# Optimization experiments

Measured on AMD Instinct MI355X. Metric: run time of the kernel, lower is better.

## Reference

```python
import jax, jax.numpy as jnp
import numpy as np

NUM_EXPERTS = 8
EMBED_DIM = 1024
EXPERT_DIM = 2048
TOP_K = 2
B, T = 2, 1024


def setup_inputs() -> dict:
    key = jax.random.key(0)
    ks = jax.random.split(key, 7)
    std = 0.02
    return {
        "x": jax.random.normal(ks[0], (B, T, EMBED_DIM), dtype=jnp.float32),
        "gate_inputs": jax.random.normal(ks[1], (B, T, EMBED_DIM), dtype=jnp.float32),
        "gate_kernel": jax.random.normal(ks[2], (EMBED_DIM, NUM_EXPERTS), dtype=jnp.float32) * std,
        "per_expert_scale": jnp.ones((NUM_EXPERTS,), dtype=jnp.float32),
        "gate_proj_w": jax.random.normal(ks[3], (NUM_EXPERTS, EMBED_DIM, EXPERT_DIM), dtype=jnp.float32) * std,
        "up_proj_w": jax.random.normal(ks[4], (NUM_EXPERTS, EMBED_DIM, EXPERT_DIM), dtype=jnp.float32) * std,
        "down_proj_w": jax.random.normal(ks[5], (NUM_EXPERTS, EXPERT_DIM, EMBED_DIM), dtype=jnp.float32) * std,
    }


def reference(x, gate_inputs, gate_kernel, per_expert_scale,
              gate_proj_w, up_proj_w, down_proj_w):
    Bb, Tt, D = x.shape
    x_flat = x.reshape(Bb * Tt, D)          # [t, e]
    g_flat = gate_inputs.reshape(Bb * Tt, D)

    logits = jnp.dot(g_flat, gate_kernel)   # [t, n]
    topk_logits, topk_idx = jax.lax.top_k(logits, TOP_K)  # [t, k]
    weights = jax.nn.sigmoid(topk_logits)   # [t, k]

    # Dense all-expert projections (as in the original module)
    gate_out = jnp.einsum('te,ned->tnd', x_flat, gate_proj_w)  # [t, n, d]
    up_out = jnp.einsum('te,ned->tnd', x_flat, up_proj_w)
    act = jax.nn.gelu(gate_out) * up_out
    expert_out = jnp.einsum('tnd,nde->tne', act, down_proj_w)  # [t, n, e]
    expert_out = expert_out * per_expert_scale[None, :, None]

    mask = jax.nn.one_hot(topk_idx, NUM_EXPERTS, dtype=expert_out.dtype)  # [t, k, n]
    selected = jnp.einsum('tkn,tne->tke', mask, expert_out)               # [t, k, e]
    out = jnp.einsum('tk,tke->te', weights, selected)                     # [t, e]
    return out.reshape(Bb, Tt, D)
```

## Files before the change

### kernel.cpp

```cpp
#include <hip/hip_runtime.h>
#include <math.h>
#include <stdint.h>

#define NE 8
#define ED 1024
#define FD 2048
#define NTOK 2048
#define BM 128
#define BN 128
#define BK 64

typedef unsigned short u16;
typedef unsigned int u32;
typedef __attribute__((ext_vector_type(4))) float f32x4;
typedef __attribute__((ext_vector_type(8))) short s16x8;
typedef __attribute__((ext_vector_type(4))) unsigned int u32v4;


__device__ __forceinline__ u16 f2bf(float f) {
    u32 u = __builtin_bit_cast(u32, f);
    u32 r = u + 0x7fffu + ((u >> 16) & 1u);
    return (u16)(r >> 16);
}

typedef __attribute__((address_space(1))) const void gvoid_t;
typedef __attribute__((address_space(3))) void lvoid_t;

__device__ __forceinline__ void gload16(const void* g, void* l) {
    __builtin_amdgcn_global_load_lds((gvoid_t*)g, (lvoid_t*)l, 16, 0, 0);
}


#define WS_CNT 0u
#define WS_OFF 64u
#define WS_TOK 256u
#define WS_WT  65792u
#define WS_XB  131328u
#define WS_WG  (8u << 20)
#define WS_WU  41943040u
#define WS_WD  75497472u
#define WS_ACT 109051904u
#define WS_NEED 130023424u


__global__ __launch_bounds__(256) void k_router(
        const float* __restrict__ gin, const float* __restrict__ gk,
        int* __restrict__ cnt, int* __restrict__ tok, float* __restrict__ wl) {
    int lane = threadIdx.x & 63;
    int t = (blockIdx.x * 256 + threadIdx.x) >> 6;
    if (t >= NTOK) return;
    const float* row = gin + (size_t)t * ED;
    float acc[NE];
#pragma unroll
    for (int e = 0; e < NE; e++) acc[e] = 0.f;
    for (int i = lane; i < ED; i += 64) {
        float v = row[i];
        const float* g = gk + i * NE;
#pragma unroll
        for (int e = 0; e < NE; e++) acc[e] = fmaf(v, g[e], acc[e]);
    }
#pragma unroll
    for (int e = 0; e < NE; e++) {
#pragma unroll
        for (int off = 32; off > 0; off >>= 1)
            acc[e] += __shfl_down(acc[e], off, 64);
    }
    if (lane == 0) {
        int b0 = 0; float v0 = acc[0];
#pragma unroll
        for (int e = 1; e < NE; e++) if (acc[e] > v0) { v0 = acc[e]; b0 = e; }
        int b1 = -1; float v1 = -3.4e38f;
#pragma unroll
        for (int e = 0; e < NE; e++) if (e != b0 && acc[e] > v1) { v1 = acc[e]; b1 = e; }
        float w0 = 1.f / (1.f + __expf(-v0));
        float w1 = 1.f / (1.f + __expf(-v1));
        int p0 = atomicAdd(&cnt[b0], 1);
        tok[b0 * NTOK + p0] = t; wl[b0 * NTOK + p0] = w0;
        int p1 = atomicAdd(&cnt[b1], 1);
        tok[b1 * NTOK + p1] = t; wl[b1 * NTOK + p1] = w1;
    }
}

__global__ void k_scan(const int* __restrict__ cnt, int* __restrict__ off) {
    if (threadIdx.x == 0 && blockIdx.x == 0) {
        int a = 0;
#pragma unroll
        for (int e = 0; e < NE; e++) { off[e] = a; a += (cnt[e] + 127) & ~127; }
        off[NE] = a;
    }
}


__global__ __launch_bounds__(256) void k_cvtx(const float4* __restrict__ x, uint2* __restrict__ xb) {
    int i = blockIdx.x * 256 + threadIdx.x;
    float4 v = x[i];
    uint2 o;
    o.x = (u32)f2bf(v.x) | ((u32)f2bf(v.y) << 16);
    o.y = (u32)f2bf(v.z) | ((u32)f2bf(v.w) << 16);
    xb[i] = o;
}


__global__ __launch_bounds__(256, 4) void k_cvtw(
        const float* __restrict__ wgf, const float* __restrict__ wuf, const float* __restrict__ wdf,
        u16* __restrict__ og, u16* __restrict__ ou, u16* __restrict__ od) {
    int b = blockIdx.x;
    const float* src; u16* dst; int ROW; int e, s;
    if (b < 1024)      { src = wgf; dst = og; ROW = FD; e = b >> 7;  s = b & 127; }
    else if (b < 2048) { int b2 = b - 1024; src = wuf; dst = ou; ROW = FD; e = b2 >> 7; s = b2 & 127; }
    else               { int b2 = b - 2048; src = wdf; dst = od; ROW = ED; e = b2 >> 8; s = b2 & 255; }
    int kc = s >> 3, g = s & 7;
    int rpe = (ROW == FD) ? ED : FD;
    const float* base = src + (size_t)e * (size_t)rpe * ROW + (size_t)s * 8 * ROW;

    __shared__ u32 sl[4 * 2052];
    int tid = threadIdx.x;
    int chunks = ROW >> 10;

    for (int kp = 0; kp < 4; kp++) {
        const float* r0 = base + (size_t)(2 * kp) * ROW;
        for (int ch = 0; ch < chunks; ch++) {
            int n4 = ch * 256 + tid;
            float4 f0 = *((const float4*)r0 + n4);
            float4 f1 = *((const float4*)(r0 + ROW) + n4);
            u32v4 w;
            w.x = (u32)f2bf(f0.x) | ((u32)f2bf(f1.x) << 16);
            w.y = (u32)f2bf(f0.y) | ((u32)f2bf(f1.y) << 16);
            w.z = (u32)f2bf(f0.z) | ((u32)f2bf(f1.z) << 16);
            w.w = (u32)f2bf(f0.w) | ((u32)f2bf(f1.w) << 16);
            *(u32v4*)(sl + kp * 2052 + 4 * n4) = w;
        }
    }
    __syncthreads();

    int iters = ROW >> 8;
    for (int it = 0; it < iters; it++) {
        int n = it * 256 + tid;
        u32v4 w;
        w.x = sl[0 * 2052 + n];
        w.y = sl[1 * 2052 + n];
        w.z = sl[2 * 2052 + n];
        w.w = sl[3 * 2052 + n];
        int nt = n >> 7;
        int img = (ROW == FD) ? ((e * 16 + nt) * 16 + kc)
                              : ((e * 8 + nt) * 32 + kc);
        u16* ob = dst + (size_t)img * 8192 + (size_t)g * 1024 + (size_t)(n & 127) * 8;
        *(u32v4*)ob = w;
    }
}


__global__ __launch_bounds__(256, 2) void k_passA(
        const u16* __restrict__ xb, const u16* __restrict__ wg, const u16* __restrict__ wu,
        const int* __restrict__ cnt, const int* __restrict__ off,
        const int* __restrict__ tok, u16* __restrict__ act) {
    int e = blockIdx.z, mt = blockIdx.y, nt = blockIdx.x;
    int c = cnt[e];
    if (mt * BM >= c) return;
    int rmax = c - mt * BM; if (rmax > BM) rmax = BM;

    __shared__ u16 sA[BM * BK];
    __shared__ u16 sBg[BN * BK];
    __shared__ u16 sBu[BN * BK];

    int tid = threadIdx.x;
    int lane = tid & 63, wv = tid >> 6;
    int wm = wv >> 1, wn = wv & 1;
    int col = lane & 15, quad = lane >> 4;
    int swz = col & 7;

    f32x4 zero = {0.f, 0.f, 0.f, 0.f};
    f32x4 ag[4][4], au[4][4];
#pragma unroll
    for (int i = 0; i < 4; i++)
#pragma unroll
        for (int j = 0; j < 4; j++) { ag[i][j] = zero; au[i][j] = zero; }

    int am = tid >> 1, ah = tid & 1;
    int ridx = mt * BM + am; if (ridx > c - 1) ridx = c - 1;
    int trow = tok[e * NTOK + ridx];
    const u16* asrc = xb + (size_t)trow * ED + ah * 32;
    u16* adst = sA + am * BK;

    const u16* gg = wg + ((size_t)(e * 16 + nt) * 16) * 8192;
    const u16* gu = wu + ((size_t)(e * 16 + nt) * 16) * 8192;
    const u16* bsrc0 = (wv < 2 ? gg : gu);
    int bhalf = (wv & 1) * 4096;
    u16* bdst = (wv < 2 ? sBg : sBu) + bhalf;

    for (int kc = 0; kc < 16; kc++) {
        __syncthreads();
        const u16* bs = bsrc0 + (size_t)kc * 8192 + bhalf + lane * 8;
#pragma unroll
        for (int i = 0; i < 8; i++)
            gload16(bs + i * 512, bdst + i * 512);
        const u16* as = asrc + kc * 64;
#pragma unroll
        for (int j = 0; j < 4; j++) {
            int pg = (ah * 4 + j) ^ (am & 7);
            *(u32v4*)(adst + pg * 8) = *(const u32v4*)(as + j * 8);
        }
        __syncthreads();
#pragma unroll
        for (int st = 0; st < 2; st++) {
            int g4 = st * 4 + quad;
            int aoff = (g4 ^ swz) * 8;
            s16x8 af[4];
#pragma unroll
            for (int mf = 0; mf < 4; mf++)
                af[mf] = *(const s16x8*)(sA + (wm * 64 + mf * 16 + col) * BK + aoff);
#pragma unroll
            for (int nf = 0; nf < 4; nf++) {
                int boff = g4 * 1024 + (wn * 64 + nf * 16 + col) * 8;
                s16x8 bg = *(const s16x8*)(sBg + boff);
                s16x8 bu = *(const s16x8*)(sBu + boff);
#pragma unroll
                for (int mf = 0; mf < 4; mf++) {
                    ag[mf][nf] = __builtin_amdgcn_mfma_f32_16x16x32_bf16(af[mf], bg, ag[mf][nf], 0, 0, 0);
                    au[mf][nf] = __builtin_amdgcn_mfma_f32_16x16x32_bf16(af[mf], bu, au[mf][nf], 0, 0, 0);
                }
            }
        }
    }

    int tile = (off[e] >> 7) + mt;
    u16* ab = act + (size_t)tile * (32 * 8192);
#pragma unroll
    for (int mf = 0; mf < 4; mf++) {
#pragma unroll
        for (int reg = 0; reg < 4; reg++) {
            int m = wm * 64 + mf * 16 + quad * 4 + reg;
            if (m < rmax) {
#pragma unroll
                for (int nf = 0; nf < 4; nf++) {
                    float gv = ag[mf][nf][reg];
                    float uv = au[mf][nf][reg];
                    float z = 0.7978845608028654f * (gv + 0.044715f * gv * gv * gv);
                    float ez = __expf(-2.f * fabsf(z));
                    float th = (1.f - ez) / (1.f + ez);
                    th = (z < 0.f) ? -th : th;
                    float a = 0.5f * gv * (1.f + th) * uv;
                    int ng = nt * 128 + wn * 64 + nf * 16 + col;
                    ab[(size_t)(ng >> 6) * 8192 + (size_t)((ng >> 3) & 7) * 1024
                       + (size_t)m * 8 + (ng & 7)] = f2bf(a);
                }
            }
        }
    }
}


__global__ __launch_bounds__(256, 3) void k_passB(
        const u16* __restrict__ act, const u16* __restrict__ wd,
        const int* __restrict__ cnt, const int* __restrict__ off,
        const int* __restrict__ tok, const float* __restrict__ wl,
        const float* __restrict__ scale, float* __restrict__ out) {
    int e = blockIdx.z, mt = blockIdx.y, nt = blockIdx.x;
    int c = cnt[e];
    if (mt * BM >= c) return;
    int rmax = c - mt * BM; if (rmax > BM) rmax = BM;

    __shared__ u16 sA[BM * BK];
    __shared__ u16 sB[BN * BK];

    int tid = threadIdx.x;
    int lane = tid & 63, wv = tid >> 6;
    int wm = wv >> 1, wn = wv & 1;
    int col = lane & 15, quad = lane >> 4;

    f32x4 zero = {0.f, 0.f, 0.f, 0.f};
    f32x4 acc[4][4];
#pragma unroll
    for (int i = 0; i < 4; i++)
#pragma unroll
        for (int j = 0; j < 4; j++) acc[i][j] = zero;

    int tile = (off[e] >> 7) + mt;
    const u16* ga = act + (size_t)tile * (32 * 8192);
    const u16* gb = wd + ((size_t)(e * 8 + nt) * 32) * 8192;
    const u16* src0 = (wv < 2 ? ga : gb);
    int shalf = (wv & 1) * 4096;
    u16* dst0 = (wv < 2 ? sA : sB) + shalf;

    for (int kc = 0; kc < 32; kc++) {
        __syncthreads();
        const u16* s = src0 + (size_t)kc * 8192 + shalf + lane * 8;
#pragma unroll
        for (int i = 0; i < 8; i++)
            gload16(s + i * 512, dst0 + i * 512);
        __syncthreads();
#pragma unroll
        for (int st = 0; st < 2; st++) {
            int g4 = st * 4 + quad;
            int abase = g4 * 1024;
            s16x8 af[4];
#pragma unroll
            for (int mf = 0; mf < 4; mf++)
                af[mf] = *(const s16x8*)(sA + abase + (wm * 64 + mf * 16 + col) * 8);
#pragma unroll
            for (int nf = 0; nf < 4; nf++) {
                s16x8 bf = *(const s16x8*)(sB + abase + (wn * 64 + nf * 16 + col) * 8);
#pragma unroll
                for (int mf = 0; mf < 4; mf++)
                    acc[mf][nf] = __builtin_amdgcn_mfma_f32_16x16x32_bf16(af[mf], bf, acc[mf][nf], 0, 0, 0);
            }
        }
    }

    float sc = scale[e];
    int lbase = e * NTOK + mt * BM;
#pragma unroll
    for (int mf = 0; mf < 4; mf++) {
#pragma unroll
        for (int reg = 0; reg < 4; reg++) {
            int m = wm * 64 + mf * 16 + quad * 4 + reg;
            if (m < rmax) {
                int t = tok[lbase + m];
                float w = wl[lbase + m] * sc;
                float* orow = out + (size_t)t * ED + nt * 128 + wn * 64 + col;
#pragma unroll
                for (int nf = 0; nf < 4; nf++)
                    atomicAdd(orow + nf * 16, acc[mf][nf][reg] * w);
            }
        }
    }
}


extern "C" void kernel_launch(void* const* d_in, const int* in_sizes, int n_in,
                              void* d_out, int out_size, void* d_ws, size_t ws_size,
                              hipStream_t stream) {
    const float* x   = (const float*)d_in[0];
    const float* gin = (const float*)d_in[1];
    const float* gk  = (const float*)d_in[2];
    const float* sc  = (const float*)d_in[3];
    const float* wgf = (const float*)d_in[4];
    const float* wuf = (const float*)d_in[5];
    const float* wdf = (const float*)d_in[6];
    float* out = (float*)d_out;

    if (ws_size < (size_t)WS_NEED) {
        hipMemsetAsync(d_out, 0, (size_t)out_size * sizeof(float), stream);
        return;
    }

    char* ws = (char*)d_ws;
    int*   cnt = (int*)(ws + WS_CNT);
    int*   off = (int*)(ws + WS_OFF);
    int*   tok = (int*)(ws + WS_TOK);
    float* wl  = (float*)(ws + WS_WT);
    u16*   xb  = (u16*)(ws + WS_XB);
    u16*   og  = (u16*)(ws + WS_WG);
    u16*   ou  = (u16*)(ws + WS_WU);
    u16*   od  = (u16*)(ws + WS_WD);
    u16*   act = (u16*)(ws + WS_ACT);

    hipMemsetAsync(cnt, 0, 64, stream);
    hipMemsetAsync(d_out, 0, (size_t)out_size * sizeof(float), stream);

    k_router<<<dim3(512), dim3(256), 0, stream>>>(gin, gk, cnt, tok, wl);
    k_scan<<<dim3(1), dim3(64), 0, stream>>>(cnt, off);
    k_cvtx<<<dim3(2048), dim3(256), 0, stream>>>((const float4*)x, (uint2*)xb);
    k_cvtw<<<dim3(4096), dim3(256), 0, stream>>>(wgf, wuf, wdf, og, ou, od);
    k_passA<<<dim3(16, 16, NE), dim3(256), 0, stream>>>(xb, og, ou, cnt, off, tok, act);
    k_passB<<<dim3(8, 16, NE), dim3(256), 0, stream>>>(act, od, cnt, off, tok, wl, sc, out);
}
```

Before: 429.2 us.

## Fuse router and conversions into one prep kernel, overlap down-weight conversion with passA

Merges the router, x conversion and gate/up weight conversion kernels into a single k_prep launch, which cuts launch count and tail gaps between them. The down-projection weight conversion moves into extra blocks of k_passA (grid z doubled), so it runs alongside the gate/up GEMM instead of before it. The cost is shared LDS sizing and branch divergence across block roles, and conversion blocks may compete with GEMM blocks for occupancy and bandwidth.

```diff
diff --git a/kernel.cpp b/kernel.cpp
--- a/kernel.cpp
+++ b/kernel.cpp
@@ -42,45 +42,6 @@
 #define WS_ACT 109051904u
 #define WS_NEED 130023424u
 
-
-__global__ __launch_bounds__(256) void k_router(
-        const float* __restrict__ gin, const float* __restrict__ gk,
-        int* __restrict__ cnt, int* __restrict__ tok, float* __restrict__ wl) {
-    int lane = threadIdx.x & 63;
-    int t = (blockIdx.x * 256 + threadIdx.x) >> 6;
-    if (t >= NTOK) return;
-    const float* row = gin + (size_t)t * ED;
-    float acc[NE];
-#pragma unroll
-    for (int e = 0; e < NE; e++) acc[e] = 0.f;
-    for (int i = lane; i < ED; i += 64) {
-        float v = row[i];
-        const float* g = gk + i * NE;
-#pragma unroll
-        for (int e = 0; e < NE; e++) acc[e] = fmaf(v, g[e], acc[e]);
-    }
-#pragma unroll
-    for (int e = 0; e < NE; e++) {
-#pragma unroll
-        for (int off = 32; off > 0; off >>= 1)
-            acc[e] += __shfl_down(acc[e], off, 64);
-    }
-    if (lane == 0) {
-        int b0 = 0; float v0 = acc[0];
-#pragma unroll
-        for (int e = 1; e < NE; e++) if (acc[e] > v0) { v0 = acc[e]; b0 = e; }
-        int b1 = -1; float v1 = -3.4e38f;
-#pragma unroll
-        for (int e = 0; e < NE; e++) if (e != b0 && acc[e] > v1) { v1 = acc[e]; b1 = e; }
-        float w0 = 1.f / (1.f + __expf(-v0));
-        float w1 = 1.f / (1.f + __expf(-v1));
-        int p0 = atomicAdd(&cnt[b0], 1);
-        tok[b0 * NTOK + p0] = t; wl[b0 * NTOK + p0] = w0;
-        int p1 = atomicAdd(&cnt[b1], 1);
-        tok[b1 * NTOK + p1] = t; wl[b1 * NTOK + p1] = w1;
-    }
-}
-
 __global__ void k_scan(const int* __restrict__ cnt, int* __restrict__ off) {
     if (threadIdx.x == 0 && blockIdx.x == 0) {
         int a = 0;
@@ -91,79 +52,156 @@
 }
 
 
-__global__ __launch_bounds__(256) void k_cvtx(const float4* __restrict__ x, uint2* __restrict__ xb) {
-    int i = blockIdx.x * 256 + threadIdx.x;
-    float4 v = x[i];
-    uint2 o;
-    o.x = (u32)f2bf(v.x) | ((u32)f2bf(v.y) << 16);
-    o.y = (u32)f2bf(v.z) | ((u32)f2bf(v.w) << 16);
-    xb[i] = o;
-}
-
-
-__global__ __launch_bounds__(256, 4) void k_cvtw(
-        const float* __restrict__ wgf, const float* __restrict__ wuf, const float* __restrict__ wdf,
-        u16* __restrict__ og, u16* __restrict__ ou, u16* __restrict__ od) {
-    int b = blockIdx.x;
-    const float* src; u16* dst; int ROW; int e, s;
-    if (b < 1024)      { src = wgf; dst = og; ROW = FD; e = b >> 7;  s = b & 127; }
-    else if (b < 2048) { int b2 = b - 1024; src = wuf; dst = ou; ROW = FD; e = b2 >> 7; s = b2 & 127; }
-    else               { int b2 = b - 2048; src = wdf; dst = od; ROW = ED; e = b2 >> 8; s = b2 & 255; }
-    int kc = s >> 3, g = s & 7;
-    int rpe = (ROW == FD) ? ED : FD;
-    const float* base = src + (size_t)e * (size_t)rpe * ROW + (size_t)s * 8 * ROW;
-
+__global__ __launch_bounds__(256, 4) void k_prep(
+        const float* __restrict__ gin, const float* __restrict__ gk,
+        const float4* __restrict__ x,
+        const float* __restrict__ wgf, const float* __restrict__ wuf,
+        int* __restrict__ cnt, int* __restrict__ tok, float* __restrict__ wl,
+        uint2* __restrict__ xb, u16* __restrict__ og, u16* __restrict__ ou) {
     __shared__ u32 sl[4 * 2052];
+    int blk = blockIdx.x;
     int tid = threadIdx.x;
-    int chunks = ROW >> 10;
-
-    for (int kp = 0; kp < 4; kp++) {
-        const float* r0 = base + (size_t)(2 * kp) * ROW;
-        for (int ch = 0; ch < chunks; ch++) {
-            int n4 = ch * 256 + tid;
+
+    if (blk < 512) {
+        int lane = tid & 63;
+        int t = (blk * 256 + tid) >> 6;
+        const float* row = gin + (size_t)t * ED;
+        float acc[NE];
+#pragma unroll
+        for (int e = 0; e < NE; e++) acc[e] = 0.f;
+        for (int i = lane; i < ED; i += 64) {
+            float v = row[i];
+            const float* g = gk + i * NE;
+#pragma unroll
+            for (int e = 0; e < NE; e++) acc[e] = fmaf(v, g[e], acc[e]);
+        }
+#pragma unroll
+        for (int e = 0; e < NE; e++) {
+#pragma unroll
+            for (int off = 32; off > 0; off >>= 1)
+                acc[e] += __shfl_down(acc[e], off, 64);
+        }
+        if (lane == 0) {
+            int b0 = 0; float v0 = acc[0];
+#pragma unroll
+            for (int e = 1; e < NE; e++) if (acc[e] > v0) { v0 = acc[e]; b0 = e; }
+            int b1 = -1; float v1 = -3.4e38f;
+#pragma unroll
+            for (int e = 0; e < NE; e++) if (e != b0 && acc[e] > v1) { v1 = acc[e]; b1 = e; }
+            float w0 = 1.f / (1.f + __expf(-v0));
+            float w1 = 1.f / (1.f + __expf(-v1));
+            int p0 = atomicAdd(&cnt[b0], 1);
+            tok[b0 * NTOK + p0] = t; wl[b0 * NTOK + p0] = w0;
+            int p1 = atomicAdd(&cnt[b1], 1);
+            tok[b1 * NTOK + p1] = t; wl[b1 * NTOK + p1] = w1;
+        }
+        return;
+    }
+
+    if (blk < 2560) {
+        int i = (blk - 512) * 256 + tid;
+        float4 v = x[i];
+        uint2 o;
+        o.x = (u32)f2bf(v.x) | ((u32)f2bf(v.y) << 16);
+        o.y = (u32)f2bf(v.z) | ((u32)f2bf(v.w) << 16);
+        xb[i] = o;
+        return;
+    }
+
+    {
+        int b = blk - 2560;
+        const float* src; u16* dst;
+        int e, s;
+        if (b < 1024) { src = wgf; dst = og; e = b >> 7; s = b & 127; }
+        else          { int b2 = b - 1024; src = wuf; dst = ou; e = b2 >> 7; s = b2 & 127; }
+        int kc = s >> 3, g = s & 7;
+        const float* base = src + (size_t)e * (size_t)ED * FD + (size_t)s * 8 * FD;
+
+        for (int kp = 0; kp < 4; kp++) {
+            const float* r0 = base + (size_t)(2 * kp) * FD;
+#pragma unroll
+            for (int ch = 0; ch < 2; ch++) {
+                int n4 = ch * 256 + tid;
+                float4 f0 = *((const float4*)r0 + n4);
+                float4 f1 = *((const float4*)(r0 + FD) + n4);
+                u32v4 w;
+                w.x = (u32)f2bf(f0.x) | ((u32)f2bf(f1.x) << 16);
+                w.y = (u32)f2bf(f0.y) | ((u32)f2bf(f1.y) << 16);
+                w.z = (u32)f2bf(f0.z) | ((u32)f2bf(f1.z) << 16);
+                w.w = (u32)f2bf(f0.w) | ((u32)f2bf(f1.w) << 16);
+                *(u32v4*)(sl + kp * 2052 + 4 * n4) = w;
+            }
+        }
+        __syncthreads();
+
+#pragma unroll
+        for (int it = 0; it < 8; it++) {
+            int n = it * 256 + tid;
+            u32v4 w;
+            w.x = sl[0 * 2052 + n];
+            w.y = sl[1 * 2052 + n];
+            w.z = sl[2 * 2052 + n];
+            w.w = sl[3 * 2052 + n];
+            int nt = n >> 7;
+            int img = (e * 16 + nt) * 16 + kc;
+            u16* ob = dst + (size_t)img * 8192 + (size_t)g * 1024 + (size_t)(n & 127) * 8;
+            *(u32v4*)ob = w;
+        }
+    }
+}
+
+
+__global__ __launch_bounds__(256, 2) void k_passA(
+        const u16* __restrict__ xb, const u16* __restrict__ wg, const u16* __restrict__ wu,
+        const float* __restrict__ wdf, u16* __restrict__ od,
+        const int* __restrict__ cnt, const int* __restrict__ off,
+        const int* __restrict__ tok, u16* __restrict__ act) {
+    __shared__ __align__(16) u16 smem[3 * 8192];
+    int tid = threadIdx.x;
+
+    if (blockIdx.z >= 8) {
+        int cid = (int)((blockIdx.z - 8) * 256 + blockIdx.y * 16 + blockIdx.x);
+        int e = cid >> 8, s = cid & 255;
+        int kc = s >> 3, g = s & 7;
+        const float* base = wdf + (size_t)e * (size_t)FD * ED + (size_t)s * 8 * ED;
+        u32* sl = (u32*)smem;
+        for (int kp = 0; kp < 4; kp++) {
+            const float* r0 = base + (size_t)(2 * kp) * ED;
+            int n4 = tid;
             float4 f0 = *((const float4*)r0 + n4);
-            float4 f1 = *((const float4*)(r0 + ROW) + n4);
+            float4 f1 = *((const float4*)(r0 + ED) + n4);
             u32v4 w;
             w.x = (u32)f2bf(f0.x) | ((u32)f2bf(f1.x) << 16);
             w.y = (u32)f2bf(f0.y) | ((u32)f2bf(f1.y) << 16);
             w.z = (u32)f2bf(f0.z) | ((u32)f2bf(f1.z) << 16);
             w.w = (u32)f2bf(f0.w) | ((u32)f2bf(f1.w) << 16);
-            *(u32v4*)(sl + kp * 2052 + 4 * n4) = w;
-        }
-    }
-    __syncthreads();
-
-    int iters = ROW >> 8;
-    for (int it = 0; it < iters; it++) {
-        int n = it * 256 + tid;
-        u32v4 w;
-        w.x = sl[0 * 2052 + n];
-        w.y = sl[1 * 2052 + n];
-        w.z = sl[2 * 2052 + n];
-        w.w = sl[3 * 2052 + n];
-        int nt = n >> 7;
-        int img = (ROW == FD) ? ((e * 16 + nt) * 16 + kc)
-                              : ((e * 8 + nt) * 32 + kc);
-        u16* ob = dst + (size_t)img * 8192 + (size_t)g * 1024 + (size_t)(n & 127) * 8;
-        *(u32v4*)ob = w;
-    }
-}
-
-
-__global__ __launch_bounds__(256, 2) void k_passA(
-        const u16* __restrict__ xb, const u16* __restrict__ wg, const u16* __restrict__ wu,
-        const int* __restrict__ cnt, const int* __restrict__ off,
-        const int* __restrict__ tok, u16* __restrict__ act) {
+            *(u32v4*)(sl + kp * 1028 + 4 * n4) = w;
+        }
+        __syncthreads();
+#pragma unroll
+        for (int it = 0; it < 4; it++) {
+            int n = it * 256 + tid;
+            u32v4 w;
+            w.x = sl[0 * 1028 + n];
+            w.y = sl[1 * 1028 + n];
+            w.z = sl[2 * 1028 + n];
+            w.w = sl[3 * 1028 + n];
+            int nt = n >> 7;
+            int img = (e * 8 + nt) * 32 + kc;
+            *(u32v4*)(od + (size_t)img * 8192 + (size_t)g * 1024 + (size_t)(n & 127) * 8) = w;
+        }
+        return;
+    }
+
     int e = blockIdx.z, mt = blockIdx.y, nt = blockIdx.x;
     int c = cnt[e];
     if (mt * BM >= c) return;
     int rmax = c - mt * BM; if (rmax > BM) rmax = BM;
 
-    __shared__ u16 sA[BM * BK];
-    __shared__ u16 sBg[BN * BK];
-    __shared__ u16 sBu[BN * BK];
-
-    int tid = threadIdx.x;
+    u16* sA  = smem;
+    u16* sBg = smem + 8192;
+    u16* sBu = smem + 16384;
+
     int lane = tid & 63, wv = tid >> 6;
     int wm = wv >> 1, wn = wv & 1;
     int col = lane & 15, quad = lane >> 4;
@@ -358,10 +396,11 @@
     hipMemsetAsync(cnt, 0, 64, stream);
     hipMemsetAsync(d_out, 0, (size_t)out_size * sizeof(float), stream);
 
-    k_router<<<dim3(512), dim3(256), 0, stream>>>(gin, gk, cnt, tok, wl);
+    k_prep<<<dim3(4608), dim3(256), 0, stream>>>(gin, gk, (const float4*)x,
+                                                 wgf, wuf, cnt, tok, wl,
+                                                 (uint2*)xb, og, ou);
     k_scan<<<dim3(1), dim3(64), 0, stream>>>(cnt, off);
-    k_cvtx<<<dim3(2048), dim3(256), 0, stream>>>((const float4*)x, (uint2*)xb);
-    k_cvtw<<<dim3(4096), dim3(256), 0, stream>>>(wgf, wuf, wdf, og, ou, od);
-    k_passA<<<dim3(16, 16, NE), dim3(256), 0, stream>>>(xb, og, ou, cnt, off, tok, act);
+    k_passA<<<dim3(16, 16, 16), dim3(256), 0, stream>>>(xb, og, ou, wdf, od,
+                                                        cnt, off, tok, act);
     k_passB<<<dim3(8, 16, NE), dim3(256), 0, stream>>>(act, od, cnt, off, tok, wl, sc, out);
 }
```

After: 393.2 us. 8.4% less time.

## Fuse weight bf16 conversion into expert GEMM loads and merge router with x conversion

Applied to the files above, without the earlier changes.

Removes the standalone weight-conversion kernel: passA and passB now load fp32 weights directly, convert them to bf16 in registers and write the packed layout into shared memory. The router and x-conversion kernels are merged into one launch. This is meant to eliminate the round-trip write and re-read of a ~100MB bf16 weight copy and a launch. In exchange, each GEMM block reads twice the bytes per weight tile and does conversion ALU work inside the main loop, and weight tiles are re-read in fp32 by every m-tile.

```diff
diff --git a/kernel.cpp b/kernel.cpp
--- a/kernel.cpp
+++ b/kernel.cpp
@@ -23,6 +23,10 @@
     return (u16)(r >> 16);
 }
 
+__device__ __forceinline__ u32 pk2(float a, float b) {
+    return (u32)f2bf(a) | ((u32)f2bf(b) << 16);
+}
+
 typedef __attribute__((address_space(1))) const void gvoid_t;
 typedef __attribute__((address_space(3))) void lvoid_t;
 
@@ -36,50 +40,8 @@
 #define WS_TOK 256u
 #define WS_WT  65792u
 #define WS_XB  131328u
-#define WS_WG  (8u << 20)
-#define WS_WU  41943040u
-#define WS_WD  75497472u
-#define WS_ACT 109051904u
-#define WS_NEED 130023424u
-
-
-__global__ __launch_bounds__(256) void k_router(
-        const float* __restrict__ gin, const float* __restrict__ gk,
-        int* __restrict__ cnt, int* __restrict__ tok, float* __restrict__ wl) {
-    int lane = threadIdx.x & 63;
-    int t = (blockIdx.x * 256 + threadIdx.x) >> 6;
-    if (t >= NTOK) return;
-    const float* row = gin + (size_t)t * ED;
-    float acc[NE];
-#pragma unroll
-    for (int e = 0; e < NE; e++) acc[e] = 0.f;
-    for (int i = lane; i < ED; i += 64) {
-        float v = row[i];
-        const float* g = gk + i * NE;
-#pragma unroll
-        for (int e = 0; e < NE; e++) acc[e] = fmaf(v, g[e], acc[e]);
-    }
-#pragma unroll
-    for (int e = 0; e < NE; e++) {
-#pragma unroll
-        for (int off = 32; off > 0; off >>= 1)
-            acc[e] += __shfl_down(acc[e], off, 64);
-    }
-    if (lane == 0) {
-        int b0 = 0; float v0 = acc[0];
-#pragma unroll
-        for (int e = 1; e < NE; e++) if (acc[e] > v0) { v0 = acc[e]; b0 = e; }
-        int b1 = -1; float v1 = -3.4e38f;
-#pragma unroll
-        for (int e = 0; e < NE; e++) if (e != b0 && acc[e] > v1) { v1 = acc[e]; b1 = e; }
-        float w0 = 1.f / (1.f + __expf(-v0));
-        float w1 = 1.f / (1.f + __expf(-v1));
-        int p0 = atomicAdd(&cnt[b0], 1);
-        tok[b0 * NTOK + p0] = t; wl[b0 * NTOK + p0] = w0;
-        int p1 = atomicAdd(&cnt[b1], 1);
-        tok[b1 * NTOK + p1] = t; wl[b1 * NTOK + p1] = w1;
-    }
-}
+#define WS_ACT 4325632u
+#define WS_NEED 25297152u
 
 __global__ void k_scan(const int* __restrict__ cnt, int* __restrict__ off) {
     if (threadIdx.x == 0 && blockIdx.x == 0) {
@@ -91,67 +53,62 @@
 }
 
 
-__global__ __launch_bounds__(256) void k_cvtx(const float4* __restrict__ x, uint2* __restrict__ xb) {
-    int i = blockIdx.x * 256 + threadIdx.x;
+__global__ __launch_bounds__(256) void k_prep(
+        const float* __restrict__ gin, const float* __restrict__ gk,
+        const float4* __restrict__ x,
+        int* __restrict__ cnt, int* __restrict__ tok, float* __restrict__ wl,
+        uint2* __restrict__ xb) {
+    int blk = blockIdx.x;
+    int tid = threadIdx.x;
+
+    if (blk < 512) {
+        int lane = tid & 63;
+        int t = (blk * 256 + tid) >> 6;
+        const float* row = gin + (size_t)t * ED;
+        float acc[NE];
+#pragma unroll
+        for (int e = 0; e < NE; e++) acc[e] = 0.f;
+        for (int i = lane; i < ED; i += 64) {
+            float v = row[i];
+            const float* g = gk + i * NE;
+#pragma unroll
+            for (int e = 0; e < NE; e++) acc[e] = fmaf(v, g[e], acc[e]);
+        }
+#pragma unroll
+        for (int e = 0; e < NE; e++) {
+#pragma unroll
+            for (int off = 32; off > 0; off >>= 1)
+                acc[e] += __shfl_down(acc[e], off, 64);
+        }
+        if (lane == 0) {
+            int b0 = 0; float v0 = acc[0];
+#pragma unroll
+            for (int e = 1; e < NE; e++) if (acc[e] > v0) { v0 = acc[e]; b0 = e; }
+            int b1 = -1; float v1 = -3.4e38f;
+#pragma unroll
+            for (int e = 0; e < NE; e++) if (e != b0 && acc[e] > v1) { v1 = acc[e]; b1 = e; }
+            float w0 = 1.f / (1.f + __expf(-v0));
+            float w1 = 1.f / (1.f + __expf(-v1));
+            int p0 = atomicAdd(&cnt[b0], 1);
+            tok[b0 * NTOK + p0] = t; wl[b0 * NTOK + p0] = w0;
+            int p1 = atomicAdd(&cnt[b1], 1);
+            tok[b1 * NTOK + p1] = t; wl[b1 * NTOK + p1] = w1;
+        }
+        return;
+    }
+
+    int i = (blk - 512) * 256 + tid;
     float4 v = x[i];
     uint2 o;
-    o.x = (u32)f2bf(v.x) | ((u32)f2bf(v.y) << 16);
-    o.y = (u32)f2bf(v.z) | ((u32)f2bf(v.w) << 16);
+    o.x = pk2(v.x, v.y);
+    o.y = pk2(v.z, v.w);
     xb[i] = o;
 }
 
 
-__global__ __launch_bounds__(256, 4) void k_cvtw(
-        const float* __restrict__ wgf, const float* __restrict__ wuf, const float* __restrict__ wdf,
-        u16* __restrict__ og, u16* __restrict__ ou, u16* __restrict__ od) {
-    int b = blockIdx.x;
-    const float* src; u16* dst; int ROW; int e, s;
-    if (b < 1024)      { src = wgf; dst = og; ROW = FD; e = b >> 7;  s = b & 127; }
-    else if (b < 2048) { int b2 = b - 1024; src = wuf; dst = ou; ROW = FD; e = b2 >> 7; s = b2 & 127; }
-    else               { int b2 = b - 2048; src = wdf; dst = od; ROW = ED; e = b2 >> 8; s = b2 & 255; }
-    int kc = s >> 3, g = s & 7;
-    int rpe = (ROW == FD) ? ED : FD;
-    const float* base = src + (size_t)e * (size_t)rpe * ROW + (size_t)s * 8 * ROW;
-
-    __shared__ u32 sl[4 * 2052];
-    int tid = threadIdx.x;
-    int chunks = ROW >> 10;
-
-    for (int kp = 0; kp < 4; kp++) {
-        const float* r0 = base + (size_t)(2 * kp) * ROW;
-        for (int ch = 0; ch < chunks; ch++) {
-            int n4 = ch * 256 + tid;
-            float4 f0 = *((const float4*)r0 + n4);
-            float4 f1 = *((const float4*)(r0 + ROW) + n4);
-            u32v4 w;
-            w.x = (u32)f2bf(f0.x) | ((u32)f2bf(f1.x) << 16);
-            w.y = (u32)f2bf(f0.y) | ((u32)f2bf(f1.y) << 16);
-            w.z = (u32)f2bf(f0.z) | ((u32)f2bf(f1.z) << 16);
-            w.w = (u32)f2bf(f0.w) | ((u32)f2bf(f1.w) << 16);
-            *(u32v4*)(sl + kp * 2052 + 4 * n4) = w;
-        }
-    }
-    __syncthreads();
-
-    int iters = ROW >> 8;
-    for (int it = 0; it < iters; it++) {
-        int n = it * 256 + tid;
-        u32v4 w;
-        w.x = sl[0 * 2052 + n];
-        w.y = sl[1 * 2052 + n];
-        w.z = sl[2 * 2052 + n];
-        w.w = sl[3 * 2052 + n];
-        int nt = n >> 7;
-        int img = (ROW == FD) ? ((e * 16 + nt) * 16 + kc)
-                              : ((e * 8 + nt) * 32 + kc);
-        u16* ob = dst + (size_t)img * 8192 + (size_t)g * 1024 + (size_t)(n & 127) * 8;
-        *(u32v4*)ob = w;
-    }
-}
-
-
 __global__ __launch_bounds__(256, 2) void k_passA(
-        const u16* __restrict__ xb, const u16* __restrict__ wg, const u16* __restrict__ wu,
+        const u16* __restrict__ xb,
+        const float* __restrict__ wgf, const float* __restrict__ wuf,
         const int* __restrict__ cnt, const int* __restrict__ off,
         const int* __restrict__ tok, u16* __restrict__ act) {
     int e = blockIdx.z, mt = blockIdx.y, nt = blockIdx.x;
@@ -182,23 +139,46 @@
     const u16* asrc = xb + (size_t)trow * ED + ah * 32;
     u16* adst = sA + am * BK;
 
-    const u16* gg = wg + ((size_t)(e * 16 + nt) * 16) * 8192;
-    const u16* gu = wu + ((size_t)(e * 16 + nt) * 16) * 8192;
-    const u16* bsrc0 = (wv < 2 ? gg : gu);
-    int bhalf = (wv & 1) * 4096;
-    u16* bdst = (wv < 2 ? sBg : sBu) + bhalf;
+    int n4 = tid & 31;
+    int k8 = tid >> 5;
+    const float* gb = wgf + ((size_t)e * ED + (size_t)k8 * 8) * FD + nt * 128 + n4 * 4;
+    const float* ub = wuf + ((size_t)e * ED + (size_t)k8 * 8) * FD + nt * 128 + n4 * 4;
+    u16* bgw = sBg + (k8 * 128 + n4 * 4) * 8;
+    u16* buw = sBu + (k8 * 128 + n4 * 4) * 8;
 
     for (int kc = 0; kc < 16; kc++) {
         __syncthreads();
-        const u16* bs = bsrc0 + (size_t)kc * 8192 + bhalf + lane * 8;
-#pragma unroll
-        for (int i = 0; i < 8; i++)
-            gload16(bs + i * 512, bdst + i * 512);
+        const float* g0 = gb + (size_t)kc * 64 * FD;
+        const float* u0 = ub + (size_t)kc * 64 * FD;
+        f32x4 vg[8], vu[8];
+#pragma unroll
+        for (int r = 0; r < 8; r++) {
+            vg[r] = *(const f32x4*)(g0 + (size_t)r * FD);
+            vu[r] = *(const f32x4*)(u0 + (size_t)r * FD);
+        }
         const u16* as = asrc + kc * 64;
 #pragma unroll
         for (int j = 0; j < 4; j++) {
             int pg = (ah * 4 + j) ^ (am & 7);
             *(u32v4*)(adst + pg * 8) = *(const u32v4*)(as + j * 8);
+        }
+#pragma unroll
+        for (int j = 0; j < 4; j++) {
+            u32v4 w;
+            w.x = pk2(vg[0][j], vg[1][j]);
+            w.y = pk2(vg[2][j], vg[3][j]);
+            w.z = pk2(vg[4][j], vg[5][j]);
+            w.w = pk2(vg[6][j], vg[7][j]);
+            *(u32v4*)(bgw + j * 8) = w;
+        }
+#pragma unroll
+        for (int j = 0; j < 4; j++) {
+            u32v4 w;
+            w.x = pk2(vu[0][j], vu[1][j]);
+            w.y = pk2(vu[2][j], vu[3][j]);
+            w.z = pk2(vu[4][j], vu[5][j]);
+            w.w = pk2(vu[6][j], vu[7][j]);
+            *(u32v4*)(buw + j * 8) = w;
         }
         __syncthreads();
 #pragma unroll
@@ -251,7 +231,7 @@
 
 
 __global__ __launch_bounds__(256, 3) void k_passB(
-        const u16* __restrict__ act, const u16* __restrict__ wd,
+        const u16* __restrict__ act, const float* __restrict__ wdf,
         const int* __restrict__ cnt, const int* __restrict__ off,
         const int* __restrict__ tok, const float* __restrict__ wl,
         const float* __restrict__ scale, float* __restrict__ out) {
@@ -277,17 +257,33 @@
 
     int tile = (off[e] >> 7) + mt;
     const u16* ga = act + (size_t)tile * (32 * 8192);
-    const u16* gb = wd + ((size_t)(e * 8 + nt) * 32) * 8192;
-    const u16* src0 = (wv < 2 ? ga : gb);
-    int shalf = (wv & 1) * 4096;
-    u16* dst0 = (wv < 2 ? sA : sB) + shalf;
+
+    int n4 = tid & 31;
+    int k8 = tid >> 5;
+    const float* db = wdf + ((size_t)e * FD + (size_t)k8 * 8) * ED + nt * 128 + n4 * 4;
+    u16* bw = sB + (k8 * 128 + n4 * 4) * 8;
 
     for (int kc = 0; kc < 32; kc++) {
         __syncthreads();
-        const u16* s = src0 + (size_t)kc * 8192 + shalf + lane * 8;
-#pragma unroll
-        for (int i = 0; i < 8; i++)
-            gload16(s + i * 512, dst0 + i * 512);
+        const u16* as = ga + (size_t)kc * 8192 + wv * 2048 + lane * 8;
+        u16* ad = sA + wv * 2048 + lane * 8;
+#pragma unroll
+        for (int i = 0; i < 4; i++)
+            gload16(as + i * 512, ad + i * 512);
+        const float* d0 = db + (size_t)kc * 64 * ED;
+        f32x4 vd[8];
+#pragma unroll
+        for (int r = 0; r < 8; r++)
+            vd[r] = *(const f32x4*)(d0 + (size_t)r * ED);
+#pragma unroll
+        for (int j = 0; j < 4; j++) {
+            u32v4 w;
+            w.x = pk2(vd[0][j], vd[1][j]);
+            w.y = pk2(vd[2][j], vd[3][j]);
+            w.z = pk2(vd[4][j], vd[5][j]);
+            w.w = pk2(vd[6][j], vd[7][j]);
+            *(u32v4*)(bw + j * 8) = w;
+        }
         __syncthreads();
 #pragma unroll
         for (int st = 0; st < 2; st++) {
@@ -350,18 +346,16 @@
     int*   tok = (int*)(ws + WS_TOK);
     float* wl  = (float*)(ws + WS_WT);
     u16*   xb  = (u16*)(ws + WS_XB);
-    u16*   og  = (u16*)(ws + WS_WG);
-    u16*   ou  = (u16*)(ws + WS_WU);
-    u16*   od  = (u16*)(ws + WS_WD);
     u16*   act = (u16*)(ws + WS_ACT);
 
     hipMemsetAsync(cnt, 0, 64, stream);
     hipMemsetAsync(d_out, 0, (size_t)out_size * sizeof(float), stream);
 
-    k_router<<<dim3(512), dim3(256), 0, stream>>>(gin, gk, cnt, tok, wl);
+    k_prep<<<dim3(2560), dim3(256), 0, stream>>>(gin, gk, (const float4*)x,
+                                                 cnt, tok, wl, (uint2*)xb);
     k_scan<<<dim3(1), dim3(64), 0, stream>>>(cnt, off);
-    k_cvtx<<<dim3(2048), dim3(256), 0, stream>>>((const float4*)x, (uint2*)xb);
-    k_cvtw<<<dim3(4096), dim3(256), 0, stream>>>(wgf, wuf, wdf, og, ou, od);
-    k_passA<<<dim3(16, 16, NE), dim3(256), 0, stream>>>(xb, og, ou, cnt, off, tok, act);
-    k_passB<<<dim3(8, 16, NE), dim3(256), 0, stream>>>(act, od, cnt, off, tok, wl, sc, out);
-}
+    k_passA<<<dim3(16, 16, NE), dim3(256), 0, stream>>>(xb, wgf, wuf,
+                                                        cnt, off, tok, act);
+    k_passB<<<dim3(8, 16, NE), dim3(256), 0, stream>>>(act, wdf, cnt, off, tok,
+                                                       wl, sc, out);
+}
```

Result: slower. 640.9 us (+49.3%).
